# Kernel tuning notes

Measured on AMD Instinct MI355X. Metric: run time of the kernel, lower is better.

Reference implementation:

```python
import jax, jax.numpy as jnp
import numpy as np

B, S, H, E, K = 4, 4096, 2048, 64, 8
SEQ_ALPHA = 0.01


def setup_inputs() -> dict:
    key = jax.random.key(0)
    k1, k2 = jax.random.split(key)
    x = jax.random.normal(k1, (B, S, H), dtype=jnp.float32)
    # kaiming_uniform_(a=sqrt(5)) on [E, H] -> bound = 1/sqrt(H)
    bound = 1.0 / np.sqrt(H)
    weight = jax.random.uniform(k2, (E, H), dtype=jnp.float32, minval=-bound, maxval=bound)
    expert_bias = jnp.zeros((E,), dtype=jnp.float32)
    return {"x": x, "weight": weight, "expert_bias": expert_bias}


def reference(x, weight, expert_bias):
    bsz, seq_len, _ = x.shape
    x_flat = x.reshape(-1, x.shape[-1])                      # [T, H], T = B*S
    logits = x_flat @ weight.T                               # [T, E]
    scores = jax.nn.sigmoid(logits)
    biased_logits = logits + expert_bias[None, :]
    _, topk_idx = jax.lax.top_k(biased_logits, K)            # [T, K] int32
    topk_w = jnp.take_along_axis(scores, topk_idx, axis=-1)  # [T, K]
    topk_w = topk_w / (topk_w.sum(axis=-1, keepdims=True) + 1e-10)  # K > 1
    # load stats (training-mode bincount)
    expert_load = jnp.bincount(topk_idx.reshape(-1), length=E).astype(jnp.int64)
    # sequence-wise balance loss (DeepSeek-V3)
    scores_r = scores.reshape(bsz, seq_len, E)
    expert_mask = jax.nn.one_hot(topk_idx.reshape(bsz, -1), E, dtype=scores.dtype)  # [B, S*K, E]
    f_i = expert_mask.sum(axis=1) / (K * seq_len)            # [B, E]
    normalized = scores_r / (scores_r.sum(axis=2, keepdims=True) + 1e-10)
    P_i = normalized.mean(axis=1)                            # [B, E]
    aux_seq_loss = SEQ_ALPHA * (f_i * P_i).sum(axis=1).mean()
    return (topk_idx, topk_w, aux_seq_loss, expert_load)
```

## Files before the change

### kernel.cpp

```cpp
#include <hip/hip_runtime.h>
#include <math.h>

#define HDIM 2048
#define TTOK 16384
#define NEXP 64
#define TOPK 8
#define SLEN 4096
#define NBATCH 4
#define PARTSZ (NEXP * TTOK)

#define OFF_W    131072
#define OFF_LOSS 262144
#define OFF_LOAD 262145

#define WS_PACC 0
#define WS_CACC 8192
#define WS_WT   16384
#define WS_PART (16384 + HDIM * NEXP)
#define EPI_NBLK 256

__global__ __launch_bounds__(256) void transpose_w(const float* __restrict__ W,
                                                   float* __restrict__ Wt,
                                                   float* __restrict__ wsz) {
  __shared__ float tile[64][65];
  const int tid = threadIdx.x;
  const int k0 = blockIdx.x * 64;
  if (blockIdx.x == 0) {
    const float4 z = {0.f, 0.f, 0.f, 0.f};
    float4* wz4 = (float4*)wsz;
#pragma unroll
    for (int i = 0; i < 16; ++i) wz4[tid + (i << 8)] = z;
  }
  {
    const int kc = (tid & 15) << 2;
    const int er = tid >> 4;
#pragma unroll
    for (int i = 0; i < 4; ++i) {
      int e = er + i * 16;
      float4 v = *(const float4*)(W + (size_t)e * HDIM + k0 + kc);
      tile[e][kc + 0] = v.x; tile[e][kc + 1] = v.y;
      tile[e][kc + 2] = v.z; tile[e][kc + 3] = v.w;
    }
  }
  __syncthreads();
  {
    const int e4 = (tid & 15) << 2;
    const int kr = tid >> 4;
#pragma unroll
    for (int i = 0; i < 4; ++i) {
      int k = kr + i * 16;
      float4 v;
      v.x = tile[e4 + 0][k]; v.y = tile[e4 + 1][k];
      v.z = tile[e4 + 2][k]; v.w = tile[e4 + 3][k];
      *(float4*)(Wt + (size_t)(k0 + k) * NEXP + e4) = v;
    }
  }
}

template <int KS>
__global__ __launch_bounds__(512, 8) void gate_gemm(
    const float* __restrict__ x,
    const float* __restrict__ Wt,
    float* __restrict__ part) {
  constexpr int KR = HDIM / KS;
  constexpr int NT = KR / 32;
  __shared__ float xs[2][128 * 32];

  const int tid = threadIdx.x;
  const int lane = tid & 63;
  const int wv = __builtin_amdgcn_readfirstlane(tid >> 6);
  const int eg = wv & 3;
  const int th = wv >> 2;
  const int bid = blockIdx.x;
  const int kh = bid & (KS - 1);
  const int tg = bid >> (KS == 8 ? 3 : 2);
  const int tok0 = tg << 7;
  const int kb = kh * KR;

  float acc[16];
#pragma unroll
  for (int j = 0; j < 16; ++j) acc[j] = 0.f;

  const int r0 = tid >> 3;
  const int sg = tid & 7;
  const int sslot = (sg ^ (r0 & 7)) << 2;
  const float* xp0 = x + (size_t)(tok0 + r0) * HDIM + kb + (sg << 2);
  const float* xp1 = xp0 + (size_t)64 * HDIM;
  float4 a0 = *(const float4*)xp0;
  float4 a1 = *(const float4*)xp1;

  const int myrow = (th << 6) + lane;
  const int rbase = myrow << 5;
  const int rs = lane & 7;

  for (int kt = 0; kt < NT; ++kt) {
    float* xb = &xs[kt & 1][0];
    *(float4*)&xb[(r0 << 5) + sslot] = a0;
    *(float4*)&xb[((r0 + 64) << 5) + sslot] = a1;
    __syncthreads();
    if (kt + 1 < NT) {
      a0 = *(const float4*)(xp0 + ((kt + 1) << 5));
      a1 = *(const float4*)(xp1 + ((kt + 1) << 5));
    }
    const float* wkb = Wt + ((size_t)(kb + (kt << 5)) << 6) + (eg << 4);
#pragma unroll
    for (int c = 0; c < 8; ++c) {
      float4 xv = *(const float4*)&xb[rbase + ((c ^ rs) << 2)];
      const float xf[4] = {xv.x, xv.y, xv.z, xv.w};
#pragma unroll
      for (int q = 0; q < 4; ++q) {
        const float* wr = wkb + (((c << 2) + q) << 6);
#pragma unroll
        for (int j = 0; j < 16; ++j) acc[j] = fmaf(xf[q], wr[j], acc[j]);
      }
    }
  }

  float* dst = part + (size_t)kh * PARTSZ + ((size_t)(eg << 4)) * TTOK + tok0 +
               (th << 6) + lane;
#pragma unroll
  for (int j = 0; j < 16; ++j) dst[(size_t)j * TTOK] = acc[j];
}

#define WRED_SUM(v) { v += __shfl_xor(v, 1);  v += __shfl_xor(v, 2);  \
                      v += __shfl_xor(v, 4);  v += __shfl_xor(v, 8);  \
                      v += __shfl_xor(v, 16); v += __shfl_xor(v, 32); }
#define WRED_MAX(v) { v = fmaxf(v, __shfl_xor(v, 1));  v = fmaxf(v, __shfl_xor(v, 2));  \
                      v = fmaxf(v, __shfl_xor(v, 4));  v = fmaxf(v, __shfl_xor(v, 8));  \
                      v = fmaxf(v, __shfl_xor(v, 16)); v = fmaxf(v, __shfl_xor(v, 32)); }
#define PICK(IJ, WJ) {                                                    \
    float m_ = cand; WRED_MAX(m_);                                        \
    unsigned long long mk_ = __ballot(cand == m_);                        \
    int win_ = (int)__ffsll(mk_) - 1;                                     \
    float bw_ = __shfl(bias_r, win_);                                     \
    WJ = 1.f / (1.f + expf(-(m_ - bw_)));                                 \
    wsum += WJ; IJ = win_;                                                \
    if (lane == win_) { cand = -1e30f; cnt += 1.f; } }

template <int KS>
__global__ __launch_bounds__(512) void gate_epilogue(
    const float* __restrict__ part, const float* __restrict__ bias,
    float* __restrict__ out, float* __restrict__ Pacc,
    float* __restrict__ Cacc) {
  __shared__ float le[64 * 65];
  __shared__ float psum_sh[8][64];
  __shared__ float cnt_sh[8][64];

  const int tid = threadIdx.x;
  const int lane = tid & 63;
  const int wv = tid >> 6;
  const int t0 = blockIdx.x << 6;

  {
    const int e = tid >> 3;
    const int tsub = tid & 7;
#pragma unroll
    for (int w = 0; w < 2; ++w) {
      const int tq = (tsub << 3) + (w << 2);
      const float* p = part + (size_t)e * TTOK + t0 + tq;
      float4 v[KS];
#pragma unroll
      for (int s = 0; s < KS; ++s) v[s] = *(const float4*)(p + (size_t)s * PARTSZ);
      float4 r;
      if (KS == 8) {
        r.x = ((v[0].x + v[1].x) + (v[2].x + v[3].x)) + ((v[4].x + v[5].x) + (v[6].x + v[7].x));
        r.y = ((v[0].y + v[1].y) + (v[2].y + v[3].y)) + ((v[4].y + v[5].y) + (v[6].y + v[7].y));
        r.z = ((v[0].z + v[1].z) + (v[2].z + v[3].z)) + ((v[4].z + v[5].z) + (v[6].z + v[7].z));
        r.w = ((v[0].w + v[1].w) + (v[2].w + v[3].w)) + ((v[4].w + v[5].w) + (v[6].w + v[7].w));
      } else {
        r.x = (v[0].x + v[1].x) + (v[2].x + v[3].x);
        r.y = (v[0].y + v[1].y) + (v[2].y + v[3].y);
        r.z = (v[0].z + v[1].z) + (v[2].z + v[3].z);
        r.w = (v[0].w + v[1].w) + (v[2].w + v[3].w);
      }
      le[(tq + 0) * 65 + e] = r.x; le[(tq + 1) * 65 + e] = r.y;
      le[(tq + 2) * 65 + e] = r.z; le[(tq + 3) * 65 + e] = r.w;
    }
  }
  __syncthreads();

  const float bias_r = bias[lane];
  float p_acc = 0.f, cnt = 0.f;

  for (int t = (wv << 3); t < (wv << 3) + 8; ++t) {
    float l = le[t * 65 + lane];
    float s = 1.f / (1.f + expf(-l));
    float ss = s;
    WRED_SUM(ss);
    p_acc += s * (1.f / (ss + 1e-10f));

    float cand = l + bias_r;
    float wsum = 0.f;
    int i0, i1, i2, i3, i4, i5, i6, i7;
    float w0, w1, w2, w3, w4, w5, w6, w7;
    PICK(i0, w0); PICK(i1, w1); PICK(i2, w2); PICK(i3, w3);
    PICK(i4, w4); PICK(i5, w5); PICK(i6, w6); PICK(i7, w7);

    if (lane == 0) {
      const float inv = 1.f / (wsum + 1e-10f);
      const int t1 = t0 + t;
      float4 o;
      o.x = (float)i0; o.y = (float)i1; o.z = (float)i2; o.w = (float)i3;
      *(float4*)(out + (size_t)t1 * TOPK) = o;
      o.x = (float)i4; o.y = (float)i5; o.z = (float)i6; o.w = (float)i7;
      *(float4*)(out + (size_t)t1 * TOPK + 4) = o;
      o.x = w0 * inv; o.y = w1 * inv; o.z = w2 * inv; o.w = w3 * inv;
      *(float4*)(out + OFF_W + (size_t)t1 * TOPK) = o;
      o.x = w4 * inv; o.y = w5 * inv; o.z = w6 * inv; o.w = w7 * inv;
      *(float4*)(out + OFF_W + (size_t)t1 * TOPK + 4) = o;
    }
  }

  psum_sh[wv][lane] = p_acc;
  cnt_sh[wv][lane] = cnt;
  __syncthreads();

  if (tid < 64) {
    const int b = (int)(blockIdx.x >> 6);
    float p = 0.f, c = 0.f;
#pragma unroll
    for (int w = 0; w < 8; ++w) { p += psum_sh[w][tid]; c += cnt_sh[w][tid]; }
    atomicAdd(&Pacc[(size_t)((b << 6) + tid) << 5], p);
    atomicAdd(&Cacc[(size_t)((b << 6) + tid) << 5], c);
  }
}

__global__ __launch_bounds__(64) void gate_finalize(
    const float* __restrict__ Pacc, const float* __restrict__ Cacc,
    float* __restrict__ out) {
  const int e = threadIdx.x;
  float load = 0.f, partl = 0.f;
#pragma unroll
  for (int bb = 0; bb < NBATCH; ++bb) {
    float c = Cacc[(size_t)((bb << 6) + e) << 5];
    float p = Pacc[(size_t)((bb << 6) + e) << 5];
    load += c;
    partl += (c * (1.f / (TOPK * (float)SLEN))) * (p * (1.f / (float)SLEN));
  }
  out[OFF_LOAD + e] = load;
#pragma unroll
  for (int off = 32; off; off >>= 1) partl += __shfl_down(partl, off);
  if (e == 0) out[OFF_LOSS] = 0.01f * partl * (1.f / (float)NBATCH);
}

extern "C" void kernel_launch(void* const* d_in, const int* in_sizes, int n_in,
                              void* d_out, int out_size, void* d_ws, size_t ws_size,
                              hipStream_t stream) {
  const float* x = (const float*)d_in[0];
  const float* W = (const float*)d_in[1];
  const float* bias = (const float*)d_in[2];
  float* out = (float*)d_out;

  float* ws = (float*)d_ws;
  float* Pacc = ws + WS_PACC;
  float* Cacc = ws + WS_CACC;
  float* Wt = ws + WS_WT;
  float* part = ws + WS_PART;

  transpose_w<<<32, 256, 0, stream>>>(W, Wt, ws);

  const size_t need8 = ((size_t)WS_PART + 8 * (size_t)PARTSZ) * sizeof(float);
  if (ws_size >= need8) {
    gate_gemm<8><<<1024, 512, 0, stream>>>(x, Wt, part);
    gate_epilogue<8><<<EPI_NBLK, 512, 0, stream>>>(part, bias, out, Pacc, Cacc);
  } else {
    gate_gemm<4><<<512, 512, 0, stream>>>(x, Wt, part);
    gate_epilogue<4><<<EPI_NBLK, 512, 0, stream>>>(part, bias, out, Pacc, Cacc);
  }
  gate_finalize<<<1, 64, 0, stream>>>(Pacc, Cacc, out);
}
```

Baseline: 248.6 us.

## Replace FP32 FMA gate GEMM with split-bf16 MFMA (3-term) emulation

The gate GEMM now splits x and W into bf16 hi/lo planes and accumulates three bf16 MFMA products (hi*hi, hi*lo, lo*hi) on the matrix cores, replacing the scalar FP32 FMA loop. The weight prep kernel emits the pre-split hi/lo planes in MFMA fragment order instead of a plain transpose. The partial-sum layout changes to token-major, and the epilogue reads are adjusted to match. This trades vector-ALU FMA throughput for matrix-core throughput plus per-element split work on x. It risks small accuracy differences that could flip top-k ties.

Measured after the change: 232.9 us. -6.3%, faster.

```diff
diff --git a/kernel.cpp b/kernel.cpp
--- a/kernel.cpp
+++ b/kernel.cpp
@@ -15,111 +15,176 @@
 
 #define WS_PACC 0
 #define WS_CACC 8192
-#define WS_WT   16384
-#define WS_PART (16384 + HDIM * NEXP)
+#define WS_WF   16384
+#define WS_PART (16384 + 131072)
+#define WFLO    131072
 #define EPI_NBLK 256
 
-__global__ __launch_bounds__(256) void transpose_w(const float* __restrict__ W,
-                                                   float* __restrict__ Wt,
-                                                   float* __restrict__ wsz) {
-  __shared__ float tile[64][65];
-  const int tid = threadIdx.x;
-  const int k0 = blockIdx.x * 64;
+using s16x8 = __attribute__((ext_vector_type(8))) short;
+using f32x4 = __attribute__((ext_vector_type(4))) float;
+
+__device__ __forceinline__ unsigned bfh(float v) {
+  unsigned b = __float_as_uint(v);
+  return (b + 0x7FFFu + ((b >> 16) & 1u)) >> 16;
+}
+
+__device__ __forceinline__ void split8(const float* f, uint4* hi, uint4* lo) {
+  unsigned h[8], l[8];
+#pragma unroll
+  for (int j = 0; j < 8; ++j) {
+    h[j] = bfh(f[j]);
+    l[j] = bfh(f[j] - __uint_as_float(h[j] << 16));
+  }
+  *hi = make_uint4(h[0] | (h[1] << 16), h[2] | (h[3] << 16),
+                   h[4] | (h[5] << 16), h[6] | (h[7] << 16));
+  *lo = make_uint4(l[0] | (l[1] << 16), l[2] | (l[3] << 16),
+                   l[4] | (l[5] << 16), l[6] | (l[7] << 16));
+}
+
+__global__ __launch_bounds__(256) void prep_wf(const float* __restrict__ W,
+                                               ushort* __restrict__ WF,
+                                               float* __restrict__ wsz) {
+  const int id = blockIdx.x * 256 + threadIdx.x;
   if (blockIdx.x == 0) {
     const float4 z = {0.f, 0.f, 0.f, 0.f};
     float4* wz4 = (float4*)wsz;
 #pragma unroll
-    for (int i = 0; i < 16; ++i) wz4[tid + (i << 8)] = z;
-  }
-  {
-    const int kc = (tid & 15) << 2;
-    const int er = tid >> 4;
-#pragma unroll
-    for (int i = 0; i < 4; ++i) {
-      int e = er + i * 16;
-      float4 v = *(const float4*)(W + (size_t)e * HDIM + k0 + kc);
-      tile[e][kc + 0] = v.x; tile[e][kc + 1] = v.y;
-      tile[e][kc + 2] = v.z; tile[e][kc + 3] = v.w;
-    }
-  }
-  __syncthreads();
-  {
-    const int e4 = (tid & 15) << 2;
-    const int kr = tid >> 4;
-#pragma unroll
-    for (int i = 0; i < 4; ++i) {
-      int k = kr + i * 16;
-      float4 v;
-      v.x = tile[e4 + 0][k]; v.y = tile[e4 + 1][k];
-      v.z = tile[e4 + 2][k]; v.w = tile[e4 + 3][k];
-      *(float4*)(Wt + (size_t)(k0 + k) * NEXP + e4) = v;
-    }
-  }
+    for (int i = 0; i < 16; ++i) wz4[threadIdx.x + (i << 8)] = z;
+  }
+  const int lane = id & 63;
+  const int reg = (id >> 6) & 1;
+  const int nt = (id >> 7) & 3;
+  const int kt = (id >> 9) & 31;
+  const int plane = id >> 14;
+  const int e = (nt << 4) + (lane & 15);
+  const int k0 = (kt << 6) + (reg << 5) + ((lane >> 4) << 3);
+  const float* src = W + (size_t)e * HDIM + k0;
+  unsigned w[4];
+#pragma unroll
+  for (int j = 0; j < 4; ++j) {
+    float v0 = src[2 * j], v1 = src[2 * j + 1];
+    unsigned h0 = bfh(v0), h1 = bfh(v1);
+    if (plane) {
+      h0 = bfh(v0 - __uint_as_float(h0 << 16));
+      h1 = bfh(v1 - __uint_as_float(h1 << 16));
+    }
+    w[j] = h0 | (h1 << 16);
+  }
+  *(uint4*)(WF + ((size_t)id << 3)) = make_uint4(w[0], w[1], w[2], w[3]);
 }
 
 template <int KS>
-__global__ __launch_bounds__(512, 8) void gate_gemm(
+__global__ __launch_bounds__(512, 4) void gate_gemm(
     const float* __restrict__ x,
-    const float* __restrict__ Wt,
+    const ushort* __restrict__ WF,
     float* __restrict__ part) {
   constexpr int KR = HDIM / KS;
-  constexpr int NT = KR / 32;
-  __shared__ float xs[2][128 * 32];
+  constexpr int NTILE = KR / 64;
+  __shared__ ushort XhL[2][128 * 64];
+  __shared__ ushort XlL[2][128 * 64];
 
   const int tid = threadIdx.x;
   const int lane = tid & 63;
   const int wv = __builtin_amdgcn_readfirstlane(tid >> 6);
-  const int eg = wv & 3;
-  const int th = wv >> 2;
+  const int wtok = (wv & 3) << 5;
+  const int nt0 = (wv >> 2) << 1;
   const int bid = blockIdx.x;
   const int kh = bid & (KS - 1);
   const int tg = bid >> (KS == 8 ? 3 : 2);
   const int tok0 = tg << 7;
   const int kb = kh * KR;
-
-  float acc[16];
-#pragma unroll
-  for (int j = 0; j < 16; ++j) acc[j] = 0.f;
-
-  const int r0 = tid >> 3;
-  const int sg = tid & 7;
-  const int sslot = (sg ^ (r0 & 7)) << 2;
-  const float* xp0 = x + (size_t)(tok0 + r0) * HDIM + kb + (sg << 2);
-  const float* xp1 = xp0 + (size_t)64 * HDIM;
-  float4 a0 = *(const float4*)xp0;
-  float4 a1 = *(const float4*)xp1;
-
-  const int myrow = (th << 6) + lane;
-  const int rbase = myrow << 5;
-  const int rs = lane & 7;
-
-  for (int kt = 0; kt < NT; ++kt) {
-    float* xb = &xs[kt & 1][0];
-    *(float4*)&xb[(r0 << 5) + sslot] = a0;
-    *(float4*)&xb[((r0 + 64) << 5) + sslot] = a1;
+  const int kbw = kb >> 6;
+
+  const int fl = lane & 15, fg = lane >> 4;
+
+  const int srow = tid >> 2;
+  const int sg2 = (tid & 3) << 1;
+  const float* xsrc = x + (size_t)(tok0 + srow) * HDIM + kb + (sg2 << 3);
+  float fA[16];
+  {
+    float4 t0 = *(const float4*)xsrc;
+    float4 t1 = *(const float4*)(xsrc + 4);
+    float4 t2 = *(const float4*)(xsrc + 8);
+    float4 t3 = *(const float4*)(xsrc + 12);
+    fA[0]=t0.x; fA[1]=t0.y; fA[2]=t0.z; fA[3]=t0.w;
+    fA[4]=t1.x; fA[5]=t1.y; fA[6]=t1.z; fA[7]=t1.w;
+    fA[8]=t2.x; fA[9]=t2.y; fA[10]=t2.z; fA[11]=t2.w;
+    fA[12]=t3.x; fA[13]=t3.y; fA[14]=t3.z; fA[15]=t3.w;
+  }
+  const int wr0 = srow * 64 + (((sg2 + 0) ^ (srow & 7)) << 3);
+  const int wr1 = srow * 64 + (((sg2 + 1) ^ (srow & 7)) << 3);
+
+  f32x4 acc00 = {0.f,0.f,0.f,0.f}, acc01 = {0.f,0.f,0.f,0.f};
+  f32x4 acc10 = {0.f,0.f,0.f,0.f}, acc11 = {0.f,0.f,0.f,0.f};
+
+  const int arow0 = wtok + fl;
+  const int arow1 = wtok + 16 + fl;
+
+  for (int kt = 0; kt < NTILE; ++kt) {
+    const int buf = kt & 1;
+    {
+      uint4 h0, l0, h1, l1;
+      split8(&fA[0], &h0, &l0);
+      split8(&fA[8], &h1, &l1);
+      *(uint4*)&XhL[buf][wr0] = h0;
+      *(uint4*)&XlL[buf][wr0] = l0;
+      *(uint4*)&XhL[buf][wr1] = h1;
+      *(uint4*)&XlL[buf][wr1] = l1;
+    }
     __syncthreads();
-    if (kt + 1 < NT) {
-      a0 = *(const float4*)(xp0 + ((kt + 1) << 5));
-      a1 = *(const float4*)(xp1 + ((kt + 1) << 5));
-    }
-    const float* wkb = Wt + ((size_t)(kb + (kt << 5)) << 6) + (eg << 4);
-#pragma unroll
-    for (int c = 0; c < 8; ++c) {
-      float4 xv = *(const float4*)&xb[rbase + ((c ^ rs) << 2)];
-      const float xf[4] = {xv.x, xv.y, xv.z, xv.w};
-#pragma unroll
-      for (int q = 0; q < 4; ++q) {
-        const float* wr = wkb + (((c << 2) + q) << 6);
-#pragma unroll
-        for (int j = 0; j < 16; ++j) acc[j] = fmaf(xf[q], wr[j], acc[j]);
-      }
-    }
-  }
-
-  float* dst = part + (size_t)kh * PARTSZ + ((size_t)(eg << 4)) * TTOK + tok0 +
-               (th << 6) + lane;
-#pragma unroll
-  for (int j = 0; j < 16; ++j) dst[(size_t)j * TTOK] = acc[j];
+    if (kt + 1 < NTILE) {
+      const float* xs = xsrc + ((kt + 1) << 6);
+      float4 t0 = *(const float4*)xs;
+      float4 t1 = *(const float4*)(xs + 4);
+      float4 t2 = *(const float4*)(xs + 8);
+      float4 t3 = *(const float4*)(xs + 12);
+      fA[0]=t0.x; fA[1]=t0.y; fA[2]=t0.z; fA[3]=t0.w;
+      fA[4]=t1.x; fA[5]=t1.y; fA[6]=t1.z; fA[7]=t1.w;
+      fA[8]=t2.x; fA[9]=t2.y; fA[10]=t2.z; fA[11]=t2.w;
+      fA[12]=t3.x; fA[13]=t3.y; fA[14]=t3.z; fA[15]=t3.w;
+    }
+    const int ktW = kbw + kt;
+#pragma unroll
+    for (int ss = 0; ss < 2; ++ss) {
+      const int g = (ss << 2) + fg;
+      const int ia0 = arow0 * 64 + ((g ^ (arow0 & 7)) << 3);
+      const int ia1 = arow1 * 64 + ((g ^ (arow1 & 7)) << 3);
+      s16x8 ah0 = *(const s16x8*)&XhL[buf][ia0];
+      s16x8 al0 = *(const s16x8*)&XlL[buf][ia0];
+      s16x8 ah1 = *(const s16x8*)&XhL[buf][ia1];
+      s16x8 al1 = *(const s16x8*)&XlL[buf][ia1];
+      const size_t fb0 = ((size_t)(((ktW << 2) + nt0) * 2 + ss) << 9) + (lane << 3);
+      const size_t fb1 = ((size_t)(((ktW << 2) + nt0 + 1) * 2 + ss) << 9) + (lane << 3);
+      s16x8 bh0 = *(const s16x8*)(WF + fb0);
+      s16x8 bl0 = *(const s16x8*)(WF + WFLO + fb0);
+      s16x8 bh1 = *(const s16x8*)(WF + fb1);
+      s16x8 bl1 = *(const s16x8*)(WF + WFLO + fb1);
+      acc00 = __builtin_amdgcn_mfma_f32_16x16x32_bf16(al0, bh0, acc00, 0, 0, 0);
+      acc00 = __builtin_amdgcn_mfma_f32_16x16x32_bf16(ah0, bl0, acc00, 0, 0, 0);
+      acc00 = __builtin_amdgcn_mfma_f32_16x16x32_bf16(ah0, bh0, acc00, 0, 0, 0);
+      acc01 = __builtin_amdgcn_mfma_f32_16x16x32_bf16(al0, bh1, acc01, 0, 0, 0);
+      acc01 = __builtin_amdgcn_mfma_f32_16x16x32_bf16(ah0, bl1, acc01, 0, 0, 0);
+      acc01 = __builtin_amdgcn_mfma_f32_16x16x32_bf16(ah0, bh1, acc01, 0, 0, 0);
+      acc10 = __builtin_amdgcn_mfma_f32_16x16x32_bf16(al1, bh0, acc10, 0, 0, 0);
+      acc10 = __builtin_amdgcn_mfma_f32_16x16x32_bf16(ah1, bl0, acc10, 0, 0, 0);
+      acc10 = __builtin_amdgcn_mfma_f32_16x16x32_bf16(ah1, bh0, acc10, 0, 0, 0);
+      acc11 = __builtin_amdgcn_mfma_f32_16x16x32_bf16(al1, bh1, acc11, 0, 0, 0);
+      acc11 = __builtin_amdgcn_mfma_f32_16x16x32_bf16(ah1, bl1, acc11, 0, 0, 0);
+      acc11 = __builtin_amdgcn_mfma_f32_16x16x32_bf16(ah1, bh1, acc11, 0, 0, 0);
+    }
+  }
+
+  float* pb = part + (size_t)kh * PARTSZ;
+  const int e0 = (nt0 << 4) + fl;
+#pragma unroll
+  for (int r = 0; r < 4; ++r) {
+    const int tA = tok0 + wtok + (fg << 2) + r;
+    const int tB = tA + 16;
+    pb[(size_t)tA * 64 + e0]      = acc00[r];
+    pb[(size_t)tA * 64 + e0 + 16] = acc01[r];
+    pb[(size_t)tB * 64 + e0]      = acc10[r];
+    pb[(size_t)tB * 64 + e0 + 16] = acc11[r];
+  }
 }
 
 #define WRED_SUM(v) { v += __shfl_xor(v, 1);  v += __shfl_xor(v, 2);  \
@@ -152,15 +217,15 @@
   const int t0 = blockIdx.x << 6;
 
   {
-    const int e = tid >> 3;
-    const int tsub = tid & 7;
-#pragma unroll
-    for (int w = 0; w < 2; ++w) {
-      const int tq = (tsub << 3) + (w << 2);
-      const float* p = part + (size_t)e * TTOK + t0 + tq;
+    const int tok = tid >> 3;
+    const int eo = (tid & 7) << 3;
+    const float* p = part + (size_t)(t0 + tok) * 64 + eo;
+#pragma unroll
+    for (int h = 0; h < 2; ++h) {
       float4 v[KS];
 #pragma unroll
-      for (int s = 0; s < KS; ++s) v[s] = *(const float4*)(p + (size_t)s * PARTSZ);
+      for (int s = 0; s < KS; ++s)
+        v[s] = *(const float4*)(p + (size_t)s * PARTSZ + (h << 2));
       float4 r;
       if (KS == 8) {
         r.x = ((v[0].x + v[1].x) + (v[2].x + v[3].x)) + ((v[4].x + v[5].x) + (v[6].x + v[7].x));
@@ -173,8 +238,9 @@
         r.z = (v[0].z + v[1].z) + (v[2].z + v[3].z);
         r.w = (v[0].w + v[1].w) + (v[2].w + v[3].w);
       }
-      le[(tq + 0) * 65 + e] = r.x; le[(tq + 1) * 65 + e] = r.y;
-      le[(tq + 2) * 65 + e] = r.z; le[(tq + 3) * 65 + e] = r.w;
+      const int e = eo + (h << 2);
+      le[tok * 65 + e + 0] = r.x; le[tok * 65 + e + 1] = r.y;
+      le[tok * 65 + e + 2] = r.z; le[tok * 65 + e + 3] = r.w;
     }
   }
   __syncthreads();
@@ -254,17 +320,17 @@
   float* ws = (float*)d_ws;
   float* Pacc = ws + WS_PACC;
   float* Cacc = ws + WS_CACC;
-  float* Wt = ws + WS_WT;
+  ushort* WF = (ushort*)(ws + WS_WF);
   float* part = ws + WS_PART;
 
-  transpose_w<<<32, 256, 0, stream>>>(W, Wt, ws);
+  prep_wf<<<128, 256, 0, stream>>>(W, WF, ws);
 
   const size_t need8 = ((size_t)WS_PART + 8 * (size_t)PARTSZ) * sizeof(float);
   if (ws_size >= need8) {
-    gate_gemm<8><<<1024, 512, 0, stream>>>(x, Wt, part);
+    gate_gemm<8><<<1024, 512, 0, stream>>>(x, WF, part);
     gate_epilogue<8><<<EPI_NBLK, 512, 0, stream>>>(part, bias, out, Pacc, Cacc);
   } else {
-    gate_gemm<4><<<512, 512, 0, stream>>>(x, Wt, part);
+    gate_gemm<4><<<512, 512, 0, stream>>>(x, WF, part);
     gate_epilogue<4><<<EPI_NBLK, 512, 0, stream>>>(part, bias, out, Pacc, Cacc);
   }
   gate_finalize<<<1, 64, 0, stream>>>(Pacc, Cacc, out);
```
